# Optimization experiments

Hardware: AMD Instinct MI355X
Metric: run time of the kernel (lower is better)

The kernel has to match this reference:

```python
import jax, jax.numpy as jnp
import numpy as np

S, M, B, D, H, DH = 1024, 1024, 4, 1024, 16, 64
T = S + M


def _rel_shift(x):
    # x: [i, j, b, n] -> Transformer-XL relative shift
    i, j = x.shape[0], x.shape[1]
    zero_pad = jnp.zeros((i, 1) + x.shape[2:], x.dtype)
    x_padded = jnp.concatenate([zero_pad, x], axis=1)
    x_padded = x_padded.reshape((j + 1, i) + x.shape[2:])
    return x_padded[1:].reshape(x.shape)


def setup_inputs() -> dict:
    key = jax.random.key(0)
    ks = jax.random.split(key, 8)
    sc = 0.02
    x = jax.random.normal(ks[0], (S, B, D), jnp.float32)
    memory = jax.random.normal(ks[1], (M, B, D), jnp.float32)
    pos_emb = jax.random.normal(ks[2], (T, D), jnp.float32)
    pos_bias_u = jax.random.normal(ks[3], (H, DH), jnp.float32) * sc
    pos_bias_v = jax.random.normal(ks[4], (H, DH), jnp.float32) * sc
    W_qkv = jax.random.normal(ks[5], (D, 3 * H * DH), jnp.float32) * sc
    W_rel = jax.random.normal(ks[6], (D, H * DH), jnp.float32) * sc
    W_o = jax.random.normal(ks[7], (H * DH, D), jnp.float32) * sc
    gamma = jnp.ones((D,), jnp.float32)
    beta = jnp.zeros((D,), jnp.float32)
    # causal mask accounting for memory: query i attends keys j <= i + M
    causal = jnp.arange(T)[None, :] > (jnp.arange(S)[:, None] + M)
    mask = jnp.broadcast_to(causal[:, :, None], (S, T, B))
    return {"x": x, "pos_emb": pos_emb, "pos_bias_u": pos_bias_u,
            "pos_bias_v": pos_bias_v, "memory": memory,
            "W_qkv": W_qkv, "W_rel": W_rel, "W_o": W_o,
            "gamma": gamma, "beta": beta, "mask": mask}


def reference(x, pos_emb, pos_bias_u, pos_bias_v, memory, W_qkv, W_rel, W_o, gamma, beta, mask):
    seq_len, batch, d_model = x.shape
    num_head, d_head = pos_bias_u.shape
    scale = 1.0 / d_head ** 0.5

    c = jnp.concatenate([memory, x], axis=0)          # [T, B, D]
    total_len = c.shape[0]

    qkv = c @ W_qkv                                   # [T, B, 3*H*DH]
    q, k, v = jnp.split(qkv, 3, axis=-1)
    q = q.reshape(total_len, batch, num_head, d_head)[-seq_len:]  # [S,B,H,DH]
    k = k.reshape(total_len, batch, num_head, d_head)             # [T,B,H,DH]
    v = v.reshape(total_len, batch, num_head, d_head)             # [T,B,H,DH]
    r = (pos_emb @ W_rel).reshape(total_len, num_head, d_head)    # [T,H,DH]

    AC = jnp.einsum('ibnd,jbnd->ijbn', q + pos_bias_u, k)  # content-content
    BD = jnp.einsum('ibnd,jnd->ijbn', q + pos_bias_v, r)   # content-position
    BD = _rel_shift(BD)

    attn_score = (AC + BD) * scale                    # [S,T,B,H]
    attn_score = jnp.where(mask[:, :, :, None], -jnp.inf, attn_score)
    attn_prob = jax.nn.softmax(attn_score, axis=1)

    attn_vec = jnp.einsum('ijbn,jbnd->ibnd', attn_prob, v)
    attn_vec = attn_vec.reshape(seq_len, batch, num_head * d_head)
    attn_out = attn_vec @ W_o                         # [S,B,D]

    y = x + attn_out
    mu = jnp.mean(y, axis=-1, keepdims=True)
    var = jnp.var(y, axis=-1, keepdims=True)
    return (y - mu) / jnp.sqrt(var + 1e-5) * gamma + beta
```

## Files before the change

### kernel.cpp

```cpp
#include <hip/hip_runtime.h>
#include <math.h>
#include <cstdint>
#include <cstddef>


typedef _Float16 half_t;
typedef _Float16 half8 __attribute__((ext_vector_type(8)));
typedef _Float16 half4v __attribute__((ext_vector_type(4)));
typedef float f32x4 __attribute__((ext_vector_type(4)));

#define S_LEN 1024
#define M_LEN 1024
#define T_LEN 2048
#define BATCH 4
#define NHEAD 16

__device__ inline void async_copy16(const half_t* g, half_t* l) {
  __builtin_amdgcn_global_load_lds(
      (const __attribute__((address_space(1))) void*)g,
      (__attribute__((address_space(3))) void*)l, 16, 0, 0);
}

__global__ __launch_bounds__(256) void k_pre(const float* __restrict__ mem,
                                             const float* __restrict__ x,
                                             const float* __restrict__ pos,
                                             const float* __restrict__ Wqkv,
                                             const float* __restrict__ Wrel,
                                             const float* __restrict__ Wo,
                                             half_t* __restrict__ cbf,
                                             half_t* __restrict__ posb,
                                             half_t* __restrict__ wqkvT,
                                             half_t* __restrict__ wrelT,
                                             half_t* __restrict__ woT) {
  __shared__ float tile[64][65];
  const int bid = blockIdx.x;
  const int t = threadIdx.x;
  if (bid < 10240) {
    const int i = bid * 256 + t;
    if (i < 2097152) {
      const int off = i & 1048575;
      const int sel = i >> 20;
      const float4 v = ((const float4*)(sel ? x : mem))[off];
      const int row = off >> 8, d4 = off & 255;
      const int drow = (row & 3) * 2048 + sel * 1024 + (row >> 2);
      half4v h;
      h[0] = (half_t)v.x; h[1] = (half_t)v.y; h[2] = (half_t)v.z; h[3] = (half_t)v.w;
      ((half4v*)cbf)[(drow << 8) + d4] = h;
    } else {
      const int off = i - 2097152;
      const float4 v = ((const float4*)pos)[off];
      half4v h;
      h[0] = (half_t)v.x; h[1] = (half_t)v.y; h[2] = (half_t)v.z; h[3] = (half_t)v.w;
      ((half4v*)posb)[off] = h;
    }
    return;
  }
  const int tb = bid - 10240;
  const int bx = tb & 15, y = tb >> 4;
  const float* src; half_t* dst; int C, c0;
  if (y < 48)      { src = Wqkv; dst = wqkvT; C = 3072; c0 = y * 64; }
  else if (y < 64) { src = Wrel; dst = wrelT; C = 1024; c0 = (y - 48) * 64; }
  else             { src = Wo;   dst = woT;   C = 1024; c0 = (y - 64) * 64; }
  const int r0 = bx * 64;
  const int tx = t & 63, ty4 = t >> 6;
#pragma unroll
  for (int k = 0; k < 16; ++k) {
    int row = k * 4 + ty4;
    tile[row][tx] = src[(size_t)(r0 + row) * C + c0 + tx];
  }
  __syncthreads();
#pragma unroll
  for (int k = 0; k < 16; ++k) {
    int orow = k * 4 + ty4;
    dst[(size_t)(c0 + orow) * 1024 + r0 + tx] = (half_t)tile[tx][orow];
  }
}

__device__ inline void gemm_body(const half_t* __restrict__ A,
                                 const half_t* __restrict__ B,
                                 half_t* __restrict__ C,
                                 int N, int K, int ld, int m0, int n0,
                                 half_t (*ldsA)[64], half_t (*ldsB)[64]) {
  const int t = threadIdx.x;
  const int wave = t >> 6, lane = t & 63, quad = lane >> 4, l15 = lane & 15;
  const int wm = (wave >> 1) * 64, wn = (wave & 1) * 64;
  const int srow = lane >> 3;
  const int scol = ((lane & 7) ^ srow) * 8;
  f32x4 acc[4][4] = {};
  for (int k0 = 0; k0 < K; k0 += 64) {
    __syncthreads();
#pragma unroll
    for (int i = 0; i < 4; ++i) {
      const int r0 = (wave * 4 + i) * 8;
      async_copy16(&A[(size_t)(m0 + r0 + srow) * ld + k0 + scol], &ldsA[r0][0]);
      async_copy16(&B[(size_t)(n0 + r0 + srow) * ld + k0 + scol], &ldsB[r0][0]);
    }
    __syncthreads();
#pragma unroll
    for (int ks = 0; ks < 2; ++ks) {
      half8 af[4], bf[4];
#pragma unroll
      for (int mt = 0; mt < 4; ++mt)
        af[mt] = *(const half8*)&ldsA[wm + mt * 16 + l15][((ks * 4 + quad) ^ (l15 & 7)) * 8];
#pragma unroll
      for (int nt = 0; nt < 4; ++nt)
        bf[nt] = *(const half8*)&ldsB[wn + nt * 16 + l15][((ks * 4 + quad) ^ (l15 & 7)) * 8];
#pragma unroll
      for (int mt = 0; mt < 4; ++mt)
#pragma unroll
        for (int nt = 0; nt < 4; ++nt)
          acc[mt][nt] = __builtin_amdgcn_mfma_f32_16x16x32_f16(af[mt], bf[nt], acc[mt][nt], 0, 0, 0);
    }
  }
#pragma unroll
  for (int mt = 0; mt < 4; ++mt)
#pragma unroll
    for (int nt = 0; nt < 4; ++nt)
#pragma unroll
      for (int r = 0; r < 4; ++r) {
        const int row = m0 + wm + mt * 16 + quad * 4 + r;
        const int col = n0 + wn + nt * 16 + l15;
        C[(size_t)row * N + col] = (half_t)acc[mt][nt][r];
      }
}

#define QP_STAGE(buf_, k0_)                                                    \
  do {                                                                         \
    _Pragma("unroll") for (int i_ = 0; i_ < 4; ++i_) {                         \
      const int r0_ = wave * 32 + i_ * 8;                                      \
      async_copy16(&A[(size_t)(m0 + r0_ + srw) * 1024 + (k0_) + scl],          \
                   &ldsA[buf_][r0_][0]);                                       \
      async_copy16(&B[(size_t)(n0 + r0_ + srw) * 1024 + (k0_) + scl],          \
                   &ldsB[buf_][r0_][0]);                                       \
    }                                                                          \
  } while (0)

#define QP_COMPUTE(d_)                                                         \
  do {                                                                         \
    _Pragma("unroll") for (int ks_ = 0; ks_ < 2; ++ks_) {                      \
      half8 bf_[4];                                                            \
      _Pragma("unroll") for (int nt_ = 0; nt_ < 4; ++nt_) {                    \
        const int rw_ = wn + nt_ * 16 + l15;                                   \
        bf_[nt_] =                                                             \
            *(const half8*)&ldsB[d_][rw_][((ks_ * 4 + quad) ^ (rw_ & 7)) * 8]; \
      }                                                                        \
      half8 af_[8];                                                            \
      _Pragma("unroll") for (int mt_ = 0; mt_ < 8; ++mt_) {                    \
        const int rw_ = wm + mt_ * 16 + l15;                                   \
        af_[mt_] =                                                             \
            *(const half8*)&ldsA[d_][rw_][((ks_ * 4 + quad) ^ (rw_ & 7)) * 8]; \
      }                                                                        \
      __builtin_amdgcn_s_setprio(1);                                           \
      _Pragma("unroll") for (int mt_ = 0; mt_ < 8; ++mt_)                      \
        _Pragma("unroll") for (int nt_ = 0; nt_ < 4; ++nt_)                    \
          acc[mt_][nt_] = __builtin_amdgcn_mfma_f32_16x16x32_f16(              \
              af_[mt_], bf_[nt_], acc[mt_][nt_], 0, 0, 0);                     \
      __builtin_amdgcn_s_setprio(0);                                           \
    }                                                                          \
  } while (0)

__global__ __launch_bounds__(512, 2) void k_gemm_qkv_pos(const half_t* __restrict__ cbf,
                                                         const half_t* __restrict__ wqkvT,
                                                         half_t* __restrict__ qkv,
                                                         const half_t* __restrict__ posb,
                                                         const half_t* __restrict__ wrelT,
                                                         half_t* __restrict__ rb,
                                                         half_t* __restrict__ vT) {
  __shared__ half_t ldsA[2][256][64];
  __shared__ half_t ldsB[2][256][64];
  const int t = threadIdx.x;
  const int wave = t >> 6, lane = t & 63, quad = lane >> 4, l15 = lane & 15;
  const int bid0 = blockIdx.x;
  const int bid = (bid0 & 7) * 52 + (bid0 >> 3);
  const half_t* A; const half_t* B; half_t* C; int m0, n0, N;
  if (bid < 256) {
    A = cbf;  B = wqkvT; C = qkv; N = 2048;
    m0 = (bid & 31) * 256; n0 = (bid >> 5) * 256;
  } else if (bid < 384) {
    const int b2 = bid - 256;
    A = wqkvT + 2048 * 1024; B = cbf; C = vT; N = 8192;
    m0 = (b2 & 3) * 256; n0 = (b2 >> 2) * 256;
  } else {
    const int b2 = bid - 384;
    A = posb; B = wrelT; C = rb; N = 1024;
    m0 = (b2 & 7) * 256; n0 = (b2 >> 3) * 256;
  }
  const int srw = lane >> 3;
  const int scl = ((lane & 7) ^ srw) * 8;
  const int wm = (wave >> 2) * 128, wn = (wave & 3) * 64;

  f32x4 acc[8][4] = {};

  QP_STAGE(0, 0);
  __syncthreads();
  int d = 0;
  for (int kt = 0; kt < 15; ++kt) {
    QP_STAGE(d ^ 1, (kt + 1) * 64);
    QP_COMPUTE(d);
    __syncthreads();
    d ^= 1;
  }
  QP_COMPUTE(d);

#pragma unroll
  for (int mt = 0; mt < 8; ++mt)
#pragma unroll
    for (int nt = 0; nt < 4; ++nt)
#pragma unroll
      for (int r = 0; r < 4; ++r)
        C[(size_t)(m0 + wm + mt * 16 + quad * 4 + r) * N + n0 + wn + nt * 16 + l15] =
            (half_t)acc[mt][nt][r];
}

__global__ __launch_bounds__(256) void k_gemm_proj(const half_t* __restrict__ av,
                                                   const half_t* __restrict__ woT,
                                                   half_t* __restrict__ out0,
                                                   half_t* __restrict__ out1) {
  __shared__ half_t ldsA[128][64];
  __shared__ half_t ldsB[128][64];
  const int bid = blockIdx.x;
  const int h = bid >> 8, b2 = bid & 255;
  gemm_body(av + h * 512, woT + h * 512, h ? out1 : out0,
            1024, 512, 1024, (b2 & 31) * 128, (b2 >> 5) * 128, ldsA, ldsB);
}

__global__ __launch_bounds__(512, 4) void k_attn(const half_t* __restrict__ qkv,
                                                 const half_t* __restrict__ rbuf,
                                                 const half_t* __restrict__ vT,
                                                 const float* __restrict__ pbu,
                                                 const float* __restrict__ pbv,
                                                 half_t* __restrict__ av) {
  __shared__ __align__(16) half_t ldsK[64][64];
  __shared__ __align__(16) half_t ldsV[64][64];
  __shared__ __align__(16) half_t ldsR[256][64];
  __shared__ __align__(16) half_t ldsP[8][16][72];
  const int t = threadIdx.x;
  const int wave = t >> 6, lane = t & 63, quad = lane >> 4, l15 = lane & 15;

  const int li = blockIdx.x + 8 * blockIdx.y;
  const int c = li & 255, kr = li >> 8;
  const int xe = kr == 0 ? (c & 7) : 7 - (c & 7);
  const int bn = (c >> 3) + (kr << 5);
  const int i0 = xe * 128;
  const int b = bn >> 4, n = bn & 15;
  const int i_base = i0 + wave * 16;
  const int p0 = 896 - i0;

  half8 qu[2], qv[2];
#pragma unroll
  for (int ks = 0; ks < 2; ++ks) {
    const int dh0 = ks * 32 + quad * 8;
    const half8 qf = *(const half8*)&qkv[((size_t)(b * 2048 + M_LEN + i_base + l15)) * 2048 + n * 64 + dh0];
#pragma unroll
    for (int j = 0; j < 8; ++j) {
      const float qj = (float)qf[j];
      qu[ks][j] = (half_t)(qj + pbu[n * 64 + dh0 + j]);
      qv[ks][j] = (half_t)(qj + pbv[n * 64 + dh0 + j]);
    }
  }

  int bperm_idx[4];
  bool lo_sel[4];
#pragma unroll
  for (int r = 0; r < 4; ++r) {
    const int irow = quad * 4 + r;
    bperm_idx[r] = ((lane & 48) | ((l15 + 15 - irow) & 15)) << 2;
    lo_sel[r] = (l15 <= irow);
  }

  f32x4 oacc[4] = {};
  float lpart[4] = {0.f, 0.f, 0.f, 0.f};
  const float k1 = 0.125f * 1.44269504088896f;
  const float kC = -4.0f * 1.44269504088896f;

  const int srow = t >> 3, sc3 = t & 7;
  const int sxk = (sc3 ^ (srow & 7)) * 8;

  const int ntile = xe * 2 + 18;

  half8 kreg = *(const half8*)&qkv[((size_t)(b * 2048 + srow)) * 2048 + 1024 + n * 64 + sc3 * 8];
  half8 vreg = *(const half8*)&vT[((size_t)(n * 64 + srow)) * 8192 + b * 2048 + sc3 * 8];
  half8 rreg4[4];
  int rr4[4], rc4[4];
#pragma unroll
  for (int i = 0; i < 4; ++i) {
    const int ci = t + 512 * i;
    rr4[i] = ci >> 3; rc4[i] = ci & 7;
    const int ps = p0 + rr4[i] > 2047 ? 2047 : p0 + rr4[i];
    rreg4[i] = *(const half8*)&rbuf[(size_t)ps * 1024 + n * 64 + rc4[i] * 8];
  }
  half8 rpre;

  for (int kt = 0; kt < ntile; ++kt) {
    const int j0 = kt * 64;

    __syncthreads();
    *(half8*)&ldsK[srow][sxk] = kreg;
    *(half8*)&ldsV[srow][sxk] = vreg;
    if (kt == 0) {
#pragma unroll
      for (int i = 0; i < 4; ++i) {
        const int pg = p0 + rr4[i];
        *(half8*)&ldsR[pg & 255][(rc4[i] ^ (pg & 7)) * 8] = rreg4[i];
      }
    } else {
      const int pw = j0 + p0 + 192 + srow;
      *(half8*)&ldsR[pw & 255][(sc3 ^ (pw & 7)) * 8] = rpre;
    }
    __syncthreads();

    if (kt + 1 < ntile) {
      const int j0n = j0 + 64;
      kreg = *(const half8*)&qkv[((size_t)(b * 2048 + j0n + srow)) * 2048 + 1024 + n * 64 + sc3 * 8];
      vreg = *(const half8*)&vT[((size_t)(n * 64 + srow)) * 8192 + b * 2048 + j0n + sc3 * 8];
      const int pn = j0 + p0 + 256 + srow;
      const int pc = pn > 2047 ? 2047 : pn;
      rpre = *(const half8*)&rbuf[(size_t)pc * 1024 + n * 64 + sc3 * 8];
    }

    f32x4 ac[4] = {};
#pragma unroll
    for (int ks = 0; ks < 2; ++ks)
#pragma unroll
      for (int nt = 0; nt < 4; ++nt) {
        const int row = nt * 16 + l15;
        const half8 kf = *(const half8*)&ldsK[row][((ks * 4 + quad) ^ (row & 7)) * 8];
        ac[nt] = __builtin_amdgcn_mfma_f32_16x16x32_f16(qu[ks], kf, ac[nt], 0, 0, 0);
      }

    const int rbg = j0 + p0 + 112 - wave * 16;
    f32x4 ea[5] = {};
#pragma unroll
    for (int ks = 0; ks < 2; ++ks)
#pragma unroll
      for (int et = 0; et < 5; ++et) {
        const int pr = rbg + et * 16 + l15;
        const half8 rf = *(const half8*)&ldsR[pr & 255][((ks * 4 + quad) ^ (pr & 7)) * 8];
        ea[et] = __builtin_amdgcn_mfma_f32_16x16x32_f16(qv[ks], rf, ea[et], 0, 0, 0);
      }

    const bool maskt = j0 > i_base + 960;
#pragma unroll
    for (int r = 0; r < 4; ++r) {
      const int irow = quad * 4 + r;
      const int ig = i_base + irow;
      float rot[5];
#pragma unroll
      for (int et = 0; et < 5; ++et)
        rot[et] = __int_as_float(
            __builtin_amdgcn_ds_bpermute(bperm_idx[r], __float_as_int(ea[et][r])));
      float psum = 0.f;
#pragma unroll
      for (int nt = 0; nt < 4; ++nt) {
        const float ev = lo_sel[r] ? rot[nt] : rot[nt + 1];
        const int cj = nt * 16 + l15;
        float p = __builtin_amdgcn_exp2f(fmaf(ac[nt][r] + ev, k1, kC));
        if (maskt && (j0 + cj > ig + M_LEN)) p = 0.f;
        psum += p;
        ldsP[wave][irow][cj] = (half_t)p;
      }
      lpart[r] += psum;
    }
    __builtin_amdgcn_wave_barrier();

    half8 pa[2];
#pragma unroll
    for (int ks = 0; ks < 2; ++ks)
      pa[ks] = *(const half8*)&ldsP[wave][l15][ks * 32 + quad * 8];
#pragma unroll
    for (int ks = 0; ks < 2; ++ks)
#pragma unroll
      for (int dnt = 0; dnt < 4; ++dnt) {
        const int row = dnt * 16 + l15;
        const half8 vf = *(const half8*)&ldsV[row][((ks * 4 + quad) ^ (row & 7)) * 8];
        oacc[dnt] = __builtin_amdgcn_mfma_f32_16x16x32_f16(pa[ks], vf, oacc[dnt], 0, 0, 0);
      }
  }

#pragma unroll
  for (int r = 0; r < 4; ++r) {
    float l = lpart[r];
#pragma unroll
    for (int off = 1; off < 16; off <<= 1) l += __shfl_xor(l, off);
    const float inv = 1.0f / l;
    const int ig = i_base + quad * 4 + r;
#pragma unroll
    for (int dnt = 0; dnt < 4; ++dnt)
      av[((size_t)ig * BATCH + b) * 1024 + n * 64 + dnt * 16 + l15] = (half_t)(oacc[dnt][r] * inv);
  }
}

__global__ __launch_bounds__(256) void k_ln(const float* __restrict__ x,
                                            const half_t* __restrict__ ao0,
                                            const half_t* __restrict__ ao1,
                                            const float* __restrict__ gamma,
                                            const float* __restrict__ beta,
                                            float* __restrict__ out) {
  const int row = blockIdx.x;
  const int t = threadIdx.x;
  const float4 xv = ((const float4*)(x + (size_t)row * 1024))[t];
  const half4v a4 = ((const half4v*)(ao0 + (size_t)row * 1024))[t];
  const half4v b4 = ((const half4v*)(ao1 + (size_t)row * 1024))[t];
  const float y0 = xv.x + (float)a4[0] + (float)b4[0];
  const float y1 = xv.y + (float)a4[1] + (float)b4[1];
  const float y2 = xv.z + (float)a4[2] + (float)b4[2];
  const float y3 = xv.w + (float)a4[3] + (float)b4[3];
  float s = y0 + y1 + y2 + y3;
  float ss = y0 * y0 + y1 * y1 + y2 * y2 + y3 * y3;
#pragma unroll
  for (int off = 1; off < 64; off <<= 1) {
    s += __shfl_xor(s, off);
    ss += __shfl_xor(ss, off);
  }
  __shared__ float sb[4], ssb[4];
  if ((t & 63) == 0) { sb[t >> 6] = s; ssb[t >> 6] = ss; }
  __syncthreads();
  s = sb[0] + sb[1] + sb[2] + sb[3];
  ss = ssb[0] + ssb[1] + ssb[2] + ssb[3];
  const float mean = s * (1.f / 1024.f);
  const float var = ss * (1.f / 1024.f) - mean * mean;
  const float rstd = rsqrtf(var + 1e-5f);
  const float4 g = ((const float4*)gamma)[t];
  const float4 be = ((const float4*)beta)[t];
  float4 o;
  o.x = (y0 - mean) * rstd * g.x + be.x;
  o.y = (y1 - mean) * rstd * g.y + be.y;
  o.z = (y2 - mean) * rstd * g.z + be.z;
  o.w = (y3 - mean) * rstd * g.w + be.w;
  ((float4*)(out + (size_t)row * 1024))[t] = o;
}

extern "C" void kernel_launch(void* const* d_in, const int* in_sizes, int n_in,
                              void* d_out, int out_size, void* d_ws, size_t ws_size,
                              hipStream_t stream) {
  const float* x     = (const float*)d_in[0];
  const float* pos   = (const float*)d_in[1];
  const float* pbu   = (const float*)d_in[2];
  const float* pbv   = (const float*)d_in[3];
  const float* mem   = (const float*)d_in[4];
  const float* Wqkv  = (const float*)d_in[5];
  const float* Wrel  = (const float*)d_in[6];
  const float* Wo    = (const float*)d_in[7];
  const float* gamma = (const float*)d_in[8];
  const float* beta  = (const float*)d_in[9];
  float* out = (float*)d_out;

  half_t* ws    = (half_t*)d_ws;
  half_t* cbf   = ws;
  half_t* posb  = cbf + 8388608;
  half_t* wqkvT = posb + 2097152;
  half_t* wrelT = wqkvT + 3145728;
  half_t* woT   = wrelT + 1048576;
  half_t* qkv   = woT + 1048576;
  half_t* rb    = qkv + 16777216;
  half_t* vT    = rb + 2097152;
  half_t* av    = vT + 8388608;
  half_t* aout0 = qkv;
  half_t* aout1 = qkv + 4194304;

  k_pre<<<11520, 256, 0, stream>>>(mem, x, pos, Wqkv, Wrel, Wo, cbf, posb, wqkvT, wrelT, woT);
  k_gemm_qkv_pos<<<416, 512, 0, stream>>>(cbf, wqkvT, qkv, posb, wrelT, rb, vT);
  k_attn<<<dim3(8, 64), 512, 0, stream>>>(qkv, rb, vT, pbu, pbv, av);
  k_gemm_proj<<<512, 256, 0, stream>>>(av, woT, aout0, aout1);
  k_ln<<<4096, 256, 0, stream>>>(x, aout0, aout1, gamma, beta, out);
}
```

Measured before the change: 308.4 us.

## Restructure output projection GEMM with double-buffered LDS and larger tiles

Replaces the single-buffered 128x128 output-projection GEMM with a 512-thread, 128x256-tile kernel that stages the next K slice into a second LDS buffer while computing the current one. The block index is remapped across XCD-like groups, and MFMA sections are wrapped in s_setprio. This removes the sync-load-sync bubble and halves the block count, at the cost of more LDS per block and fewer blocks (256) for the GPU's CUs.

```diff
diff --git a/kernel.cpp b/kernel.cpp
--- a/kernel.cpp
+++ b/kernel.cpp
@@ -76,54 +76,6 @@
   }
 }
 
-__device__ inline void gemm_body(const half_t* __restrict__ A,
-                                 const half_t* __restrict__ B,
-                                 half_t* __restrict__ C,
-                                 int N, int K, int ld, int m0, int n0,
-                                 half_t (*ldsA)[64], half_t (*ldsB)[64]) {
-  const int t = threadIdx.x;
-  const int wave = t >> 6, lane = t & 63, quad = lane >> 4, l15 = lane & 15;
-  const int wm = (wave >> 1) * 64, wn = (wave & 1) * 64;
-  const int srow = lane >> 3;
-  const int scol = ((lane & 7) ^ srow) * 8;
-  f32x4 acc[4][4] = {};
-  for (int k0 = 0; k0 < K; k0 += 64) {
-    __syncthreads();
-#pragma unroll
-    for (int i = 0; i < 4; ++i) {
-      const int r0 = (wave * 4 + i) * 8;
-      async_copy16(&A[(size_t)(m0 + r0 + srow) * ld + k0 + scol], &ldsA[r0][0]);
-      async_copy16(&B[(size_t)(n0 + r0 + srow) * ld + k0 + scol], &ldsB[r0][0]);
-    }
-    __syncthreads();
-#pragma unroll
-    for (int ks = 0; ks < 2; ++ks) {
-      half8 af[4], bf[4];
-#pragma unroll
-      for (int mt = 0; mt < 4; ++mt)
-        af[mt] = *(const half8*)&ldsA[wm + mt * 16 + l15][((ks * 4 + quad) ^ (l15 & 7)) * 8];
-#pragma unroll
-      for (int nt = 0; nt < 4; ++nt)
-        bf[nt] = *(const half8*)&ldsB[wn + nt * 16 + l15][((ks * 4 + quad) ^ (l15 & 7)) * 8];
-#pragma unroll
-      for (int mt = 0; mt < 4; ++mt)
-#pragma unroll
-        for (int nt = 0; nt < 4; ++nt)
-          acc[mt][nt] = __builtin_amdgcn_mfma_f32_16x16x32_f16(af[mt], bf[nt], acc[mt][nt], 0, 0, 0);
-    }
-  }
-#pragma unroll
-  for (int mt = 0; mt < 4; ++mt)
-#pragma unroll
-    for (int nt = 0; nt < 4; ++nt)
-#pragma unroll
-      for (int r = 0; r < 4; ++r) {
-        const int row = m0 + wm + mt * 16 + quad * 4 + r;
-        const int col = n0 + wn + nt * 16 + l15;
-        C[(size_t)row * N + col] = (half_t)acc[mt][nt][r];
-      }
-}
-
 #define QP_STAGE(buf_, k0_)                                                    \
   do {                                                                         \
     _Pragma("unroll") for (int i_ = 0; i_ < 4; ++i_) {                         \
@@ -212,16 +164,84 @@
             (half_t)acc[mt][nt][r];
 }
 
-__global__ __launch_bounds__(256) void k_gemm_proj(const half_t* __restrict__ av,
-                                                   const half_t* __restrict__ woT,
-                                                   half_t* __restrict__ out0,
-                                                   half_t* __restrict__ out1) {
-  __shared__ half_t ldsA[128][64];
-  __shared__ half_t ldsB[128][64];
-  const int bid = blockIdx.x;
-  const int h = bid >> 8, b2 = bid & 255;
-  gemm_body(av + h * 512, woT + h * 512, h ? out1 : out0,
-            1024, 512, 1024, (b2 & 31) * 128, (b2 >> 5) * 128, ldsA, ldsB);
+#define PJ_STAGE(buf_, k0_)                                                    \
+  do {                                                                         \
+    _Pragma("unroll") for (int i_ = 0; i_ < 2; ++i_) {                         \
+      const int r0_ = wave * 16 + i_ * 8;                                      \
+      async_copy16(&A[(size_t)(m0 + r0_ + srw) * 1024 + (k0_) + scl],          \
+                   &pA[buf_][r0_][0]);                                         \
+    }                                                                          \
+    _Pragma("unroll") for (int i_ = 0; i_ < 4; ++i_) {                         \
+      const int r0_ = wave * 32 + i_ * 8;                                      \
+      async_copy16(&B[(size_t)(n0 + r0_ + srw) * 1024 + (k0_) + scl],          \
+                   &pB[buf_][r0_][0]);                                         \
+    }                                                                          \
+  } while (0)
+
+#define PJ_COMPUTE(d_)                                                         \
+  do {                                                                         \
+    _Pragma("unroll") for (int ks_ = 0; ks_ < 2; ++ks_) {                      \
+      half8 bf_[4];                                                            \
+      _Pragma("unroll") for (int nt_ = 0; nt_ < 4; ++nt_) {                    \
+        const int rw_ = wn + nt_ * 16 + l15;                                   \
+        bf_[nt_] =                                                             \
+            *(const half8*)&pB[d_][rw_][((ks_ * 4 + quad) ^ (rw_ & 7)) * 8];   \
+      }                                                                        \
+      half8 af_[4];                                                            \
+      _Pragma("unroll") for (int mt_ = 0; mt_ < 4; ++mt_) {                    \
+        const int rw_ = wm + mt_ * 16 + l15;                                   \
+        af_[mt_] =                                                             \
+            *(const half8*)&pA[d_][rw_][((ks_ * 4 + quad) ^ (rw_ & 7)) * 8];   \
+      }                                                                        \
+      __builtin_amdgcn_s_setprio(1);                                           \
+      _Pragma("unroll") for (int mt_ = 0; mt_ < 4; ++mt_)                      \
+        _Pragma("unroll") for (int nt_ = 0; nt_ < 4; ++nt_)                    \
+          acc[mt_][nt_] = __builtin_amdgcn_mfma_f32_16x16x32_f16(              \
+              af_[mt_], bf_[nt_], acc[mt_][nt_], 0, 0, 0);                     \
+      __builtin_amdgcn_s_setprio(0);                                           \
+    }                                                                          \
+  } while (0)
+
+__global__ __launch_bounds__(512, 2) void k_gemm_proj(const half_t* __restrict__ av,
+                                                      const half_t* __restrict__ woT,
+                                                      half_t* __restrict__ out0,
+                                                      half_t* __restrict__ out1) {
+  __shared__ half_t pA[2][128][64];
+  __shared__ half_t pB[2][256][64];
+  const int t = threadIdx.x;
+  const int wave = t >> 6, lane = t & 63, quad = lane >> 4, l15 = lane & 15;
+  const int bid0 = blockIdx.x;
+  const int bs = (bid0 & 7) * 32 + (bid0 >> 3);
+  const int h = bs >> 7, b2 = bs & 127;
+  const int m0 = (b2 & 31) * 128, n0 = (b2 >> 5) * 256;
+  const half_t* A = av + h * 512;
+  const half_t* B = woT + h * 512;
+  half_t* C = h ? out1 : out0;
+  const int srw = lane >> 3;
+  const int scl = ((lane & 7) ^ srw) * 8;
+  const int wm = (wave >> 2) * 64, wn = (wave & 3) * 64;
+
+  f32x4 acc[4][4] = {};
+
+  PJ_STAGE(0, 0);
+  __syncthreads();
+  int d = 0;
+  for (int kt = 0; kt < 7; ++kt) {
+    PJ_STAGE(d ^ 1, (kt + 1) * 64);
+    PJ_COMPUTE(d);
+    __syncthreads();
+    d ^= 1;
+  }
+  PJ_COMPUTE(d);
+
+#pragma unroll
+  for (int mt = 0; mt < 4; ++mt)
+#pragma unroll
+    for (int nt = 0; nt < 4; ++nt)
+#pragma unroll
+      for (int r = 0; r < 4; ++r)
+        C[(size_t)(m0 + wm + mt * 16 + quad * 4 + r) * 1024 + n0 + wn + nt * 16 + l15] =
+            (half_t)acc[mt][nt][r];
 }
 
 __global__ __launch_bounds__(512, 4) void k_attn(const half_t* __restrict__ qkv,
@@ -461,6 +481,6 @@
   k_pre<<<11520, 256, 0, stream>>>(mem, x, pos, Wqkv, Wrel, Wo, cbf, posb, wqkvT, wrelT, woT);
   k_gemm_qkv_pos<<<416, 512, 0, stream>>>(cbf, wqkvT, qkv, posb, wrelT, rb, vT);
   k_attn<<<dim3(8, 64), 512, 0, stream>>>(qkv, rb, vT, pbu, pbv, av);
-  k_gemm_proj<<<512, 256, 0, stream>>>(av, woT, aout0, aout1);
+  k_gemm_proj<<<256, 512, 0, stream>>>(av, woT, aout0, aout1);
   k_ln<<<4096, 256, 0, stream>>>(x, aout0, aout1, gamma, beta, out);
 }
```

Measured after the change: 310.7 us. About the same (+0.8%).
